# Performance work log

Hardware: AMD Instinct MI355X
Metric: run time of the kernel (lower is better)

The kernel has to match this reference:

```python
import jax, jax.numpy as jnp
import numpy as np

B, T, C = 4, 2048, 1024
H = 16                      # n_head
D = C // H                  # head dim = 64
FF = 4 * C                  # 4096


def setup_inputs() -> dict:
    key = jax.random.key(0)
    ks = jax.random.split(key, 9)
    s = 0.02
    return {
        "x": jax.random.normal(ks[0], (B, T, C), dtype=jnp.float32),
        # LayerNorm params (elementwise affine, default torch init)
        "ln1_w": jnp.ones((C,), jnp.float32),
        "ln1_b": jnp.zeros((C,), jnp.float32),
        "ln2_w": jnp.ones((C,), jnp.float32),
        "ln2_b": jnp.zeros((C,), jnp.float32),
        # attention weights, torch Linear layout [out, in], bias=False
        "w_attn": jax.random.normal(ks[1], (3 * C, C), jnp.float32) * s,
        "w_proj": jax.random.normal(ks[2], (C, C), jnp.float32) * s,
        # FFN weights
        "w_fc": jax.random.normal(ks[3], (FF, C), jnp.float32) * s,
        "w_fc_proj": jax.random.normal(ks[4], (C, FF), jnp.float32) * s,
    }


def _layernorm(x, w, b, eps=1e-5):
    mu = jnp.mean(x, axis=-1, keepdims=True)
    var = jnp.var(x, axis=-1, keepdims=True)
    return (x - mu) * jax.lax.rsqrt(var + eps) * w + b


def _attn(h, w_attn, w_proj):
    qkv = jnp.einsum('btc,fc->btf', h, w_attn)        # [B,T,3C]
    q, k, v = jnp.split(qkv, 3, axis=-1)
    q = q.reshape(B, T, H, D).transpose(0, 2, 1, 3)   # [B,H,T,D]
    k = k.reshape(B, T, H, D).transpose(0, 2, 1, 3)
    v = v.reshape(B, T, H, D).transpose(0, 2, 1, 3)
    att = jnp.einsum('bhtd,bhsd->bhts', q, k) * (1.0 / np.sqrt(D))
    causal = jnp.tril(jnp.ones((T, T), dtype=bool))
    att = jnp.where(causal, att, -jnp.inf)
    att = jax.nn.softmax(att, axis=-1)
    y = jnp.einsum('bhts,bhsd->bhtd', att, v)         # [B,H,T,D]
    y = y.transpose(0, 2, 1, 3).reshape(B, T, C)
    return jnp.einsum('btc,oc->bto', y, w_proj)


def _ffn(h, w_fc, w_fc_proj):
    u = jax.nn.gelu(jnp.einsum('btc,fc->btf', h, w_fc), approximate=False)
    return jnp.einsum('btf,cf->btc', u, w_fc_proj)


def reference(x, ln1_w, ln1_b, ln2_w, ln2_b, w_attn, w_proj, w_fc, w_fc_proj):
    x = x + _attn(_layernorm(x, ln1_w, ln1_b), w_attn, w_proj)
    x = x + _ffn(_layernorm(x, ln2_w, ln2_b), w_fc, w_fc_proj)
    return x
```

## Files before the change

### kernel.cpp

```cpp
#include <hip/hip_runtime.h>
#include <hip/hip_bf16.h>

using bf16 = __hip_bfloat16;
typedef __attribute__((ext_vector_type(8))) short short8;
typedef __attribute__((ext_vector_type(4))) short sh4;
typedef __attribute__((ext_vector_type(4))) float f32x4;

#define B_ 4
#define T_ 2048
#define C_ 1024
#define H_ 16
#define FF_ 4096
#define M_TOK (B_ * T_)
#define SCALE2 0.1803368801111f

#define BARRIER() asm volatile("s_barrier" ::: "memory")
#define WAITLGKM0() asm volatile("s_waitcnt lgkmcnt(0)" ::: "memory")
#define WAITLGKM8() asm volatile("s_waitcnt lgkmcnt(8)" ::: "memory")
#define WAITVM4() asm volatile("s_waitcnt vmcnt(4)" ::: "memory")
#define WAITVM2() asm volatile("s_waitcnt vmcnt(2)" ::: "memory")
#define WAITVM0() asm volatile("s_waitcnt vmcnt(0)" ::: "memory")

__device__ __forceinline__ void gload16(const void* g, void* l) {
    __builtin_amdgcn_global_load_lds(
        (const __attribute__((address_space(1))) void*)g,
        (__attribute__((address_space(3))) void*)l, 16, 0, 0);
}

__device__ __forceinline__ float fexp2(float x) {
    float r;
    asm("v_exp_f32 %0, %1" : "=v"(r) : "v"(x));
    return r;
}

__device__ __forceinline__ float bf16bits2f(short s) {
    return __uint_as_float(((unsigned)(unsigned short)s) << 16);
}

template <int CTRL>
__device__ __forceinline__ float dpp_rotf(float x) {
    return __int_as_float(__builtin_amdgcn_update_dpp(
        0, __float_as_int(x), CTRL, 0xf, 0xf, true));
}
__device__ __forceinline__ float red16_max(float v) {
    v = fmaxf(v, dpp_rotf<0x128>(v));
    v = fmaxf(v, dpp_rotf<0x124>(v));
    v = fmaxf(v, dpp_rotf<0x122>(v));
    v = fmaxf(v, dpp_rotf<0x121>(v));
    return v;
}
__device__ __forceinline__ float red16_sum(float v) {
    v += dpp_rotf<0x128>(v);
    v += dpp_rotf<0x124>(v);
    v += dpp_rotf<0x122>(v);
    v += dpp_rotf<0x121>(v);
    return v;
}

__global__ void cvt_f32_bf16_v4(const float* __restrict__ in, bf16* __restrict__ out, int n4) {
    int i = blockIdx.x * blockDim.x + threadIdx.x;
    if (i < n4) {
        float4 v = ((const float4*)in)[i];
        sh4 o;
        bf16 b0 = __float2bfloat16(v.x), b1 = __float2bfloat16(v.y),
             b2 = __float2bfloat16(v.z), b3 = __float2bfloat16(v.w);
        o[0] = *(short*)&b0; o[1] = *(short*)&b1;
        o[2] = *(short*)&b2; o[3] = *(short*)&b3;
        ((sh4*)out)[i] = o;
    }
}

template <typename TIN>
__global__ __launch_bounds__(256) void ln_kernel(const TIN* __restrict__ x,
                                                 const float* __restrict__ w,
                                                 const float* __restrict__ b,
                                                 bf16* __restrict__ out) {
    int row = blockIdx.x;
    int t = threadIdx.x;
    float4 v;
    if constexpr (sizeof(TIN) == 4) {
        v = ((const float4*)(x + (size_t)row * C_))[t];
    } else {
        sh4 h = ((const sh4*)(x + (size_t)row * C_))[t];
        v.x = bf16bits2f(h[0]);
        v.y = bf16bits2f(h[1]);
        v.z = bf16bits2f(h[2]);
        v.w = bf16bits2f(h[3]);
    }
    float s = v.x + v.y + v.z + v.w;
    float s2 = v.x * v.x + v.y * v.y + v.z * v.z + v.w * v.w;
#pragma unroll
    for (int off = 32; off > 0; off >>= 1) {
        s += __shfl_down(s, off);
        s2 += __shfl_down(s2, off);
    }
    __shared__ float ss[4], ss2[4];
    int wave = t >> 6, lane = t & 63;
    if (lane == 0) { ss[wave] = s; ss2[wave] = s2; }
    __syncthreads();
    s = ss[0] + ss[1] + ss[2] + ss[3];
    s2 = ss2[0] + ss2[1] + ss2[2] + ss2[3];
    float mu = s * (1.f / C_);
    float var = s2 * (1.f / C_) - mu * mu;
    float rstd = rsqrtf(var + 1e-5f);
    float4 wv = ((const float4*)w)[t];
    float4 bv = ((const float4*)b)[t];
    sh4 o;
    bf16 b0 = __float2bfloat16((v.x - mu) * rstd * wv.x + bv.x);
    bf16 b1 = __float2bfloat16((v.y - mu) * rstd * wv.y + bv.y);
    bf16 b2 = __float2bfloat16((v.z - mu) * rstd * wv.z + bv.z);
    bf16 b3 = __float2bfloat16((v.w - mu) * rstd * wv.w + bv.w);
    o[0] = *(short*)&b0; o[1] = *(short*)&b1;
    o[2] = *(short*)&b2; o[3] = *(short*)&b3;
    ((sh4*)(out + (size_t)row * C_))[t] = o;
}

#define STG(ldsbase, g, grow0, k0)                                               \
    {                                                                            \
        _Pragma("unroll") for (int s_ = 0; s_ < 2; s_++) {                       \
            int row_ = s_ * 64 + wid * 8 + sr;                                   \
            gload16(g + (size_t)((grow0) + row_) * K + (k0) + ssc,               \
                    (ldsbase) + row_ * 64 + (lane & 7) * 8);                     \
        }                                                                        \
    }

#define HALF256 (128 * 64)
template <int EPI>
__global__ __launch_bounds__(512, 2) void gemm256(const bf16* __restrict__ Ag,
                                                  const bf16* __restrict__ Bg,
                                                  void* __restrict__ Cout,
                                                  int M, int N, int K) {
    __shared__ short SA[2][256 * 64];
    __shared__ short SB[2][256 * 64];

    const int nbx = N >> 8;
    const int nwg = nbx * (M >> 8);
    const int bid = blockIdx.x;
    const int cpx = nwg >> 3;
    const int swzb = (bid & 7) * cpx + (bid >> 3);
    const int m0 = (swzb / nbx) * 256;
    const int n0 = (swzb % nbx) * 256;

    const int t = threadIdx.x;
    const int wid = t >> 6, lane = t & 63;
    const int wm = wid >> 2, wn = wid & 3;
    const int lrow = lane & 15, lg = lane >> 4;
    const int swzr = (lane & 7) * 8;
    const int sr = lane >> 3;
    const int ssc = ((lane & 7) ^ sr) * 8;

    f32x4 acc[8][4];
#pragma unroll
    for (int mi = 0; mi < 8; mi++)
#pragma unroll
        for (int ni = 0; ni < 4; ni++) acc[mi][ni] = (f32x4){0.f, 0.f, 0.f, 0.f};
    short8 bfr[4][2];

    const int T = K >> 6;
    const int niter = T >> 1;

#define DSREADS256(q, buf)                                                       \
    if ((q) == 0) {                                                              \
        _Pragma("unroll") for (int ni = 0; ni < 4; ni++)                         \
        _Pragma("unroll") for (int ks = 0; ks < 2; ks++)                         \
            bfr[ni][ks] = *(const short8*)(&SB[buf][(wn * 64 + ni * 16 + lrow) * 64 + \
                                                    ((ks * 32 + lg * 8) ^ swzr)]);    \
    }                                                                            \
    _Pragma("unroll") for (int mi2 = 0; mi2 < 2; mi2++)                          \
    _Pragma("unroll") for (int ks = 0; ks < 2; ks++)                             \
        af[mi2 * 2 + ks] = *(const short8*)(&SA[buf][(wm * 128 + (2 * (q) + mi2) * 16 + lrow) * 64 + \
                                                     ((ks * 32 + lg * 8) ^ swzr)]);

#define MFMAS256(q)                                                              \
    __builtin_amdgcn_s_setprio(1);                                               \
    _Pragma("unroll") for (int ks = 0; ks < 2; ks++)                             \
    _Pragma("unroll") for (int ni = 0; ni < 4; ni++)                             \
    _Pragma("unroll") for (int mi2 = 0; mi2 < 2; mi2++)                          \
        acc[2 * (q) + mi2][ni] = __builtin_amdgcn_mfma_f32_16x16x32_bf16(        \
            af[mi2 * 2 + ks], bfr[ni][ks], acc[2 * (q) + mi2][ni], 0, 0, 0);     \
    __builtin_amdgcn_s_setprio(0);

    STG(&SA[0][0], Ag, m0, 0);
    STG(&SA[0][HALF256], Ag, m0 + 128, 0);
    STG(&SB[0][0], Bg, n0, 0);
    STG(&SB[0][HALF256], Bg, n0 + 128, 0);
    STG(&SB[1][0], Bg, n0, 64);
    STG(&SB[1][HALF256], Bg, n0 + 128, 64);
    WAITVM4();
    BARRIER();

    for (int iter = 0; iter < niter; iter++) {
        const int tt = 2 * iter;
        const int ka = (tt + 1) * 64, kb = (tt + 2) * 64, kc = (tt + 3) * 64;
        const bool s2 = (tt + 2 < T), s3 = (tt + 3 < T);
        const bool last = (iter == niter - 1);
        short8 af[4];

        DSREADS256(0, 0);
        STG(&SA[1][0], Ag, m0, ka);
        WAITLGKM8();
        BARRIER(); WAITLGKM0(); MFMAS256(0); BARRIER();
        DSREADS256(1, 0);
        STG(&SA[1][HALF256], Ag, m0 + 128, ka);
        BARRIER(); WAITLGKM0(); MFMAS256(1); BARRIER();
        DSREADS256(2, 0);
        if (s2) STG(&SB[0][0], Bg, n0, kb);
        BARRIER(); WAITLGKM0(); MFMAS256(2); BARRIER();
        DSREADS256(3, 0);
        if (s2) STG(&SB[0][HALF256], Bg, n0 + 128, kb);
        BARRIER(); WAITLGKM0(); MFMAS256(3);
        if (last) { WAITVM0(); } else { WAITVM4(); }
        BARRIER();
        DSREADS256(0, 1);
        if (s2) STG(&SA[0][0], Ag, m0, kb);
        WAITLGKM8();
        BARRIER(); WAITLGKM0(); MFMAS256(0); BARRIER();
        DSREADS256(1, 1);
        if (s2) STG(&SA[0][HALF256], Ag, m0 + 128, kb);
        BARRIER(); WAITLGKM0(); MFMAS256(1); BARRIER();
        DSREADS256(2, 1);
        if (s3) STG(&SB[1][0], Bg, n0, kc);
        BARRIER(); WAITLGKM0(); MFMAS256(2); BARRIER();
        DSREADS256(3, 1);
        if (s3) STG(&SB[1][HALF256], Bg, n0 + 128, kc);
        BARRIER(); WAITLGKM0(); MFMAS256(3);
        if (!last) WAITVM4();
        BARRIER();
    }

#pragma unroll
    for (int mi = 0; mi < 8; mi++) {
#pragma unroll
        for (int ni = 0; ni < 4; ni++) {
            int gr = m0 + wm * 128 + mi * 16 + lg * 4;
            int gc = n0 + wn * 64 + ni * 16 + lrow;
#pragma unroll
            for (int r = 0; r < 4; r++) {
                size_t gi = (size_t)(gr + r) * N + gc;
                float v = acc[mi][ni][r];
                if constexpr (EPI == 0) {
                    ((bf16*)Cout)[gi] = __float2bfloat16(v);
                } else if constexpr (EPI == 5) {
                    float vv = (gc < C_) ? v * SCALE2 : v;
                    ((bf16*)Cout)[gi] = __float2bfloat16(vv);
                } else {
                    float ge = 0.5f * v * (1.f + erff(v * 0.70710678f));
                    ((bf16*)Cout)[gi] = __float2bfloat16(ge);
                }
            }
        }
    }
}

template <int EPI>
__global__ __launch_bounds__(512, 2) void gemm256x128(const bf16* __restrict__ Ag,
                                                      const bf16* __restrict__ Bg,
                                                      void* __restrict__ Cout,
                                                      const void* __restrict__ Res,
                                                      int M, int N, int K) {
    __shared__ short SA[2][256 * 64];
    __shared__ short SB[2][128 * 64];

    const int nbx = N >> 7;
    const int nwg = nbx * (M >> 8);
    const int bid = blockIdx.x;
    const int cpx = nwg >> 3;
    const int swzb = (bid & 7) * cpx + (bid >> 3);
    const int m0 = (swzb / nbx) * 256;
    const int n0 = (swzb % nbx) * 128;

    const int t = threadIdx.x;
    const int wid = t >> 6, lane = t & 63;
    const int wm = wid >> 1, wn = wid & 1;
    const int lrow = lane & 15, lg = lane >> 4;
    const int swzr = (lane & 7) * 8;
    const int sr = lane >> 3;
    const int ssc = ((lane & 7) ^ sr) * 8;

    f32x4 acc[4][4];
#pragma unroll
    for (int mi = 0; mi < 4; mi++)
#pragma unroll
        for (int ni = 0; ni < 4; ni++) acc[mi][ni] = (f32x4){0.f, 0.f, 0.f, 0.f};
    short8 bfr[4][2];

    const int T = K >> 6;
    const int niter = T >> 1;

#define DSRX(p, buf)                                                             \
    if ((p) == 0) {                                                              \
        _Pragma("unroll") for (int ni = 0; ni < 4; ni++)                         \
        _Pragma("unroll") for (int ks = 0; ks < 2; ks++)                         \
            bfr[ni][ks] = *(const short8*)(&SB[buf][(wn * 64 + ni * 16 + lrow) * 64 + \
                                                    ((ks * 32 + lg * 8) ^ swzr)]);    \
    }                                                                            \
    _Pragma("unroll") for (int mi2 = 0; mi2 < 2; mi2++)                          \
    _Pragma("unroll") for (int ks = 0; ks < 2; ks++)                             \
        af[mi2 * 2 + ks] = *(const short8*)(&SA[buf][(wm * 64 + (2 * (p) + mi2) * 16 + lrow) * 64 + \
                                                     ((ks * 32 + lg * 8) ^ swzr)]);

#define MFX(p)                                                                   \
    __builtin_amdgcn_s_setprio(1);                                               \
    _Pragma("unroll") for (int ks = 0; ks < 2; ks++)                             \
    _Pragma("unroll") for (int ni = 0; ni < 4; ni++)                             \
    _Pragma("unroll") for (int mi2 = 0; mi2 < 2; mi2++)                          \
        acc[2 * (p) + mi2][ni] = __builtin_amdgcn_mfma_f32_16x16x32_bf16(        \
            af[mi2 * 2 + ks], bfr[ni][ks], acc[2 * (p) + mi2][ni], 0, 0, 0);     \
    __builtin_amdgcn_s_setprio(0);

    STG(&SA[0][0], Ag, m0, 0);
    STG(&SA[0][HALF256], Ag, m0 + 128, 0);
    STG(&SB[0][0], Bg, n0, 0);
    STG(&SB[1][0], Bg, n0, 64);
    WAITVM2();
    BARRIER();

    for (int iter = 0; iter < niter; iter++) {
        const int tt = 2 * iter;
        const int ka = (tt + 1) * 64, kb = (tt + 2) * 64, kc = (tt + 3) * 64;
        const bool s2 = (tt + 2 < T), s3 = (tt + 3 < T);
        const bool last = (iter == niter - 1);
        short8 af[4];

        DSRX(0, 0);
        STG(&SA[1][0], Ag, m0, ka);
        STG(&SA[1][HALF256], Ag, m0 + 128, ka);
        WAITLGKM8();
        BARRIER(); WAITLGKM0(); MFX(0); BARRIER();
        DSRX(1, 0);
        if (s2) STG(&SB[0][0], Bg, n0, kb);
        BARRIER(); WAITLGKM0(); MFX(1);
        if (last) { WAITVM0(); } else { WAITVM2(); }
        BARRIER();
        DSRX(0, 1);
        if (s2) {
            STG(&SA[0][0], Ag, m0, kb);
            STG(&SA[0][HALF256], Ag, m0 + 128, kb);
        }
        WAITLGKM8();
        BARRIER(); WAITLGKM0(); MFX(0); BARRIER();
        DSRX(1, 1);
        if (s3) STG(&SB[1][0], Bg, n0, kc);
        BARRIER(); WAITLGKM0(); MFX(1);
        if (last) { WAITVM0(); } else { WAITVM2(); }
        BARRIER();
    }

#pragma unroll
    for (int mi = 0; mi < 4; mi++) {
#pragma unroll
        for (int ni = 0; ni < 4; ni++) {
            int gr = m0 + wm * 64 + mi * 16 + lg * 4;
            int gc = n0 + wn * 64 + ni * 16 + lrow;
#pragma unroll
            for (int r = 0; r < 4; r++) {
                size_t gi = (size_t)(gr + r) * N + gc;
                float v = acc[mi][ni][r];
                if constexpr (EPI == 0) {
                    ((bf16*)Cout)[gi] = __float2bfloat16(v);
                } else if constexpr (EPI == 3) {
                    float res = ((const float*)Res)[gi];
                    ((bf16*)Cout)[gi] = __float2bfloat16(res + v);
                } else {
                    float res = __bfloat162float(((const bf16*)Res)[gi]);
                    ((float*)Cout)[gi] = res + v;
                }
            }
        }
    }
}

__global__ __launch_bounds__(256, 4) void flash_attn(const bf16* __restrict__ qk,
                                                     const bf16* __restrict__ vt,
                                                     bf16* __restrict__ y) {
    const int pi = blockIdx.x;
    const int bh = blockIdx.y;
    const int b = bh >> 4, h = bh & 15;
    const int t = threadIdx.x;
    const int wave = t >> 6, lane = t & 63;
    const int lrow = lane & 15, g = lane >> 4, lk = g * 8;

    __shared__ alignas(16) short Ks[64 * 72];
    __shared__ alignas(16) short Vs[64 * 72];
    __shared__ alignas(16) short Ps[64 * 72];

    const size_t rs = 2 * C_;
    const bf16* Qg = qk + (size_t)b * T_ * rs + h * 64;
    const bf16* Kg = Qg + C_;
    const bf16* Vg = vt + (size_t)(h * 64) * M_TOK + b * T_;

    const int srow = t >> 3;
    const int sc8 = (t & 7) * 8;

    for (int sel = 0; sel < 2; sel++) {
        const int qtb = sel ? pi : 31 - pi;
        const int q0 = qtb * 64;
        const int nkt = qtb + 1;

        short8 qf[2];
        {
            const bf16* qr = Qg + (size_t)(q0 + wave * 16 + lrow) * rs;
            qf[0] = *(const short8*)(qr + lk);
            qf[1] = *(const short8*)(qr + 32 + lk);
        }

        f32x4 o[4];
        float m[4], l[4];
#pragma unroll
        for (int ni = 0; ni < 4; ni++) o[ni] = (f32x4){0.f, 0.f, 0.f, 0.f};
#pragma unroll
        for (int r = 0; r < 4; r++) { m[r] = -1e30f; l[r] = 0.f; }

        short8 kr[2], vr[2];
#pragma unroll
        for (int p = 0; p < 2; p++) {
            int r = srow + p * 32;
            kr[p] = *(const short8*)(Kg + (size_t)r * rs + sc8);
            vr[p] = *(const short8*)(Vg + (size_t)r * M_TOK + sc8);
        }

        for (int kt = 0; kt < nkt; kt++) {
            const int s0 = kt * 64;
#pragma unroll
            for (int p = 0; p < 2; p++) {
                int r = srow + p * 32;
                *(short8*)(&Ks[r * 72 + sc8]) = kr[p];
                *(short8*)(&Vs[r * 72 + sc8]) = vr[p];
            }
            __syncthreads();
            if (kt + 1 < nkt) {
                const int s0n = (kt + 1) * 64;
#pragma unroll
                for (int p = 0; p < 2; p++) {
                    int r = srow + p * 32;
                    kr[p] = *(const short8*)(Kg + (size_t)(s0n + r) * rs + sc8);
                    vr[p] = *(const short8*)(Vg + (size_t)r * M_TOK + s0n + sc8);
                }
            }

            f32x4 s[4];
#pragma unroll
            for (int ni = 0; ni < 4; ni++) s[ni] = (f32x4){0.f, 0.f, 0.f, 0.f};
            __builtin_amdgcn_s_setprio(1);
#pragma unroll
            for (int ks = 0; ks < 2; ks++) {
#pragma unroll
                for (int ni = 0; ni < 4; ni++) {
                    short8 kf = *(const short8*)(&Ks[(ni * 16 + lrow) * 72 + ks * 32 + lk]);
                    s[ni] = __builtin_amdgcn_mfma_f32_16x16x32_bf16(qf[ks], kf, s[ni], 0, 0, 0);
                }
            }
            __builtin_amdgcn_s_setprio(0);

            if (kt == nkt - 1) {
#pragma unroll
                for (int ni = 0; ni < 4; ni++)
#pragma unroll
                    for (int r = 0; r < 4; r++) {
                        int qg = q0 + wave * 16 + g * 4 + r;
                        int kvg = s0 + ni * 16 + lrow;
                        if (kvg > qg) s[ni][r] = -1e30f;
                    }
            }

            float pm[4];
#pragma unroll
            for (int r = 0; r < 4; r++) {
                float v = fmaxf(fmaxf(s[0][r], s[1][r]), fmaxf(s[2][r], s[3][r]));
                pm[r] = red16_max(v);
            }
            float dmax = fmaxf(fmaxf(pm[0] - m[0], pm[1] - m[1]),
                               fmaxf(pm[2] - m[2], pm[3] - m[3]));
            if (!__all(dmax <= 8.f)) {
                float alpha[4];
#pragma unroll
                for (int r = 0; r < 4; r++) {
                    float mn = fmaxf(m[r], pm[r]);
                    alpha[r] = fexp2(m[r] - mn);
                    m[r] = mn;
                    l[r] *= alpha[r];
                }
#pragma unroll
                for (int ni = 0; ni < 4; ni++)
#pragma unroll
                    for (int r = 0; r < 4; r++) o[ni][r] *= alpha[r];
            }
            float rowsum[4] = {0.f, 0.f, 0.f, 0.f};
#pragma unroll
            for (int ni = 0; ni < 4; ni++) {
#pragma unroll
                for (int r = 0; r < 4; r++) {
                    float p = fexp2(s[ni][r] - m[r]);
                    rowsum[r] += p;
                    bf16 pb = __float2bfloat16(p);
                    Ps[(wave * 16 + g * 4 + r) * 72 + ni * 16 + lrow] = *(short*)&pb;
                }
            }
#pragma unroll
            for (int r = 0; r < 4; r++)
                l[r] += red16_sum(rowsum[r]);

            __builtin_amdgcn_s_setprio(1);
#pragma unroll
            for (int ks2 = 0; ks2 < 2; ks2++) {
                short8 pf = *(const short8*)(&Ps[(wave * 16 + lrow) * 72 + ks2 * 32 + lk]);
#pragma unroll
                for (int ni = 0; ni < 4; ni++) {
                    short8 vf = *(const short8*)(&Vs[(ni * 16 + lrow) * 72 + ks2 * 32 + lk]);
                    o[ni] = __builtin_amdgcn_mfma_f32_16x16x32_bf16(pf, vf, o[ni], 0, 0, 0);
                }
            }
            __builtin_amdgcn_s_setprio(0);
            __syncthreads();
        }

        float inv[4];
#pragma unroll
        for (int r = 0; r < 4; r++) inv[r] = 1.f / l[r];
#pragma unroll
        for (int ni = 0; ni < 4; ni++)
#pragma unroll
            for (int r = 0; r < 4; r++) {
                int qrow = q0 + wave * 16 + g * 4 + r;
                y[((size_t)(b * T_ + qrow)) * C_ + h * 64 + ni * 16 + lrow] =
                    __float2bfloat16(o[ni][r] * inv[r]);
            }
    }
}

extern "C" void kernel_launch(void* const* d_in, const int* in_sizes, int n_in,
                              void* d_out, int out_size, void* d_ws, size_t ws_size,
                              hipStream_t stream) {
    const float* x      = (const float*)d_in[0];
    const float* ln1w   = (const float*)d_in[1];
    const float* ln1b   = (const float*)d_in[2];
    const float* ln2w   = (const float*)d_in[3];
    const float* ln2b   = (const float*)d_in[4];
    const float* w_attn = (const float*)d_in[5];
    const float* w_proj = (const float*)d_in[6];
    const float* w_fc   = (const float*)d_in[7];
    const float* w_fcp  = (const float*)d_in[8];
    float* out = (float*)d_out;

    char* ws = (char*)d_ws;
    bf16* ln_buf  = (bf16*)(ws);
    bf16* qk_buf  = (bf16*)(ws + (16u << 20));
    bf16* vt_buf  = (bf16*)(ws + (48u << 20));
    bf16* ybuf    = (bf16*)(ws + (64u << 20));
    bf16* ubuf    = (bf16*)(ws + (16u << 20));
    bf16* x2b     = (bf16*)(ws + (80u << 20));
    bf16* wattn_h = (bf16*)(ws + (112u << 20));
    bf16* wproj_h = (bf16*)(ws + (118u << 20));
    bf16* wfc_h   = (bf16*)(ws + (120u << 20));
    bf16* wfcp_h  = (bf16*)(ws + (128u << 20));

    {
        int n1 = 3 * C_ * C_ / 4, n2 = C_ * C_ / 4, n3 = FF_ * C_ / 4, n4 = C_ * FF_ / 4;
        cvt_f32_bf16_v4<<<(n1 + 255) / 256, 256, 0, stream>>>(w_attn, wattn_h, n1);
        cvt_f32_bf16_v4<<<(n2 + 255) / 256, 256, 0, stream>>>(w_proj, wproj_h, n2);
        cvt_f32_bf16_v4<<<(n3 + 255) / 256, 256, 0, stream>>>(w_fc, wfc_h, n3);
        cvt_f32_bf16_v4<<<(n4 + 255) / 256, 256, 0, stream>>>(w_fcp, wfcp_h, n4);
    }

    ln_kernel<float><<<M_TOK, 256, 0, stream>>>(x, ln1w, ln1b, ln_buf);

    gemm256<5><<<dim3((M_TOK / 256) * (2 * C_ / 256)), 512, 0, stream>>>(
        ln_buf, wattn_h, qk_buf, M_TOK, 2 * C_, C_);

    gemm256x128<0><<<dim3((C_ / 256) * (M_TOK / 128)), 512, 0, stream>>>(
        wattn_h + (size_t)2 * C_ * C_, ln_buf, vt_buf, nullptr, C_, M_TOK, C_);

    flash_attn<<<dim3(16, B_ * H_), 256, 0, stream>>>(qk_buf, vt_buf, ybuf);

    gemm256x128<3><<<dim3((M_TOK / 256) * (C_ / 128)), 512, 0, stream>>>(
        ybuf, wproj_h, x2b, x, M_TOK, C_, C_);

    ln_kernel<bf16><<<M_TOK, 256, 0, stream>>>(x2b, ln2w, ln2b, ln_buf);

    gemm256<2><<<dim3((M_TOK / 256) * (FF_ / 256)), 512, 0, stream>>>(
        ln_buf, wfc_h, ubuf, M_TOK, FF_, C_);

    gemm256x128<4><<<dim3((M_TOK / 256) * (C_ / 128)), 512, 0, stream>>>(
        ubuf, wfcp_h, out, x2b, M_TOK, C_, FF_);
}
```

Before: 382.2 us.

## Swap MFMA operands for transposed accumulators and vectorize epilogue stores

Swaps the A/B operands of every MFMA in the GEMMs and attention so each lane's four accumulator registers hold consecutive columns of one row rather than four rows of one column. GEMM epilogues and attention output can then write packed 8-byte bf16 stores (and vector residual loads) instead of scalar 2-byte stores. In attention, each lane now owns a single query row, so the softmax max and sum become per-lane reductions plus two cross-lane shuffles instead of per-row DPP reductions, and P is written to LDS in packed form. The cost is a different register/fragment mapping that must stay consistent with the LDS read patterns, and the shuffles go through the LDS crossbar rather than DPP.

```diff
diff --git a/kernel.cpp b/kernel.cpp
--- a/kernel.cpp
+++ b/kernel.cpp
@@ -37,36 +37,20 @@
     return __uint_as_float(((unsigned)(unsigned short)s) << 16);
 }
 
-template <int CTRL>
-__device__ __forceinline__ float dpp_rotf(float x) {
-    return __int_as_float(__builtin_amdgcn_update_dpp(
-        0, __float_as_int(x), CTRL, 0xf, 0xf, true));
-}
-__device__ __forceinline__ float red16_max(float v) {
-    v = fmaxf(v, dpp_rotf<0x128>(v));
-    v = fmaxf(v, dpp_rotf<0x124>(v));
-    v = fmaxf(v, dpp_rotf<0x122>(v));
-    v = fmaxf(v, dpp_rotf<0x121>(v));
-    return v;
-}
-__device__ __forceinline__ float red16_sum(float v) {
-    v += dpp_rotf<0x128>(v);
-    v += dpp_rotf<0x124>(v);
-    v += dpp_rotf<0x122>(v);
-    v += dpp_rotf<0x121>(v);
-    return v;
+__device__ __forceinline__ unsigned bf2(float a, float b) {
+    bf16 x = __float2bfloat16(a), y = __float2bfloat16(b);
+    unsigned short ux = *(unsigned short*)&x, uy = *(unsigned short*)&y;
+    return (unsigned)ux | ((unsigned)uy << 16);
 }
 
 __global__ void cvt_f32_bf16_v4(const float* __restrict__ in, bf16* __restrict__ out, int n4) {
     int i = blockIdx.x * blockDim.x + threadIdx.x;
     if (i < n4) {
         float4 v = ((const float4*)in)[i];
-        sh4 o;
-        bf16 b0 = __float2bfloat16(v.x), b1 = __float2bfloat16(v.y),
-             b2 = __float2bfloat16(v.z), b3 = __float2bfloat16(v.w);
-        o[0] = *(short*)&b0; o[1] = *(short*)&b1;
-        o[2] = *(short*)&b2; o[3] = *(short*)&b3;
-        ((sh4*)out)[i] = o;
+        uint2 o;
+        o.x = bf2(v.x, v.y);
+        o.y = bf2(v.z, v.w);
+        ((uint2*)out)[i] = o;
     }
 }
 
@@ -105,14 +89,10 @@
     float rstd = rsqrtf(var + 1e-5f);
     float4 wv = ((const float4*)w)[t];
     float4 bv = ((const float4*)b)[t];
-    sh4 o;
-    bf16 b0 = __float2bfloat16((v.x - mu) * rstd * wv.x + bv.x);
-    bf16 b1 = __float2bfloat16((v.y - mu) * rstd * wv.y + bv.y);
-    bf16 b2 = __float2bfloat16((v.z - mu) * rstd * wv.z + bv.z);
-    bf16 b3 = __float2bfloat16((v.w - mu) * rstd * wv.w + bv.w);
-    o[0] = *(short*)&b0; o[1] = *(short*)&b1;
-    o[2] = *(short*)&b2; o[3] = *(short*)&b3;
-    ((sh4*)(out + (size_t)row * C_))[t] = o;
+    uint2 o;
+    o.x = bf2((v.x - mu) * rstd * wv.x + bv.x, (v.y - mu) * rstd * wv.y + bv.y);
+    o.y = bf2((v.z - mu) * rstd * wv.z + bv.z, (v.w - mu) * rstd * wv.w + bv.w);
+    ((uint2*)(out + (size_t)row * C_))[t] = o;
 }
 
 #define STG(ldsbase, g, grow0, k0)                                               \
@@ -177,7 +157,7 @@
     _Pragma("unroll") for (int ni = 0; ni < 4; ni++)                             \
     _Pragma("unroll") for (int mi2 = 0; mi2 < 2; mi2++)                          \
         acc[2 * (q) + mi2][ni] = __builtin_amdgcn_mfma_f32_16x16x32_bf16(        \
-            af[mi2 * 2 + ks], bfr[ni][ks], acc[2 * (q) + mi2][ni], 0, 0, 0);     \
+            bfr[ni][ks], af[mi2 * 2 + ks], acc[2 * (q) + mi2][ni], 0, 0, 0);     \
     __builtin_amdgcn_s_setprio(0);
 
     STG(&SA[0][0], Ag, m0, 0);
@@ -230,23 +210,26 @@
 
 #pragma unroll
     for (int mi = 0; mi < 8; mi++) {
+        const int gm = m0 + wm * 128 + mi * 16 + lrow;
 #pragma unroll
         for (int ni = 0; ni < 4; ni++) {
-            int gr = m0 + wm * 128 + mi * 16 + lg * 4;
-            int gc = n0 + wn * 64 + ni * 16 + lrow;
-#pragma unroll
-            for (int r = 0; r < 4; r++) {
-                size_t gi = (size_t)(gr + r) * N + gc;
-                float v = acc[mi][ni][r];
-                if constexpr (EPI == 0) {
-                    ((bf16*)Cout)[gi] = __float2bfloat16(v);
-                } else if constexpr (EPI == 5) {
-                    float vv = (gc < C_) ? v * SCALE2 : v;
-                    ((bf16*)Cout)[gi] = __float2bfloat16(vv);
-                } else {
-                    float ge = 0.5f * v * (1.f + erff(v * 0.70710678f));
-                    ((bf16*)Cout)[gi] = __float2bfloat16(ge);
-                }
+            const int gn = n0 + wn * 64 + ni * 16 + lg * 4;
+            size_t gi = (size_t)gm * N + gn;
+            f32x4 a = acc[mi][ni];
+            if constexpr (EPI == 0) {
+                uint2 o; o.x = bf2(a[0], a[1]); o.y = bf2(a[2], a[3]);
+                *(uint2*)&(((bf16*)Cout)[gi]) = o;
+            } else if constexpr (EPI == 5) {
+                float sc = (gn < C_) ? SCALE2 : 1.f;
+                uint2 o; o.x = bf2(a[0] * sc, a[1] * sc); o.y = bf2(a[2] * sc, a[3] * sc);
+                *(uint2*)&(((bf16*)Cout)[gi]) = o;
+            } else {
+                float g0 = 0.5f * a[0] * (1.f + erff(a[0] * 0.70710678f));
+                float g1 = 0.5f * a[1] * (1.f + erff(a[1] * 0.70710678f));
+                float g2 = 0.5f * a[2] * (1.f + erff(a[2] * 0.70710678f));
+                float g3 = 0.5f * a[3] * (1.f + erff(a[3] * 0.70710678f));
+                uint2 o; o.x = bf2(g0, g1); o.y = bf2(g2, g3);
+                *(uint2*)&(((bf16*)Cout)[gi]) = o;
             }
         }
     }
@@ -305,7 +288,7 @@
     _Pragma("unroll") for (int ni = 0; ni < 4; ni++)                             \
     _Pragma("unroll") for (int mi2 = 0; mi2 < 2; mi2++)                          \
         acc[2 * (p) + mi2][ni] = __builtin_amdgcn_mfma_f32_16x16x32_bf16(        \
-            af[mi2 * 2 + ks], bfr[ni][ks], acc[2 * (p) + mi2][ni], 0, 0, 0);     \
+            bfr[ni][ks], af[mi2 * 2 + ks], acc[2 * (p) + mi2][ni], 0, 0, 0);     \
     __builtin_amdgcn_s_setprio(0);
 
     STG(&SA[0][0], Ag, m0, 0);
@@ -348,23 +331,27 @@
 
 #pragma unroll
     for (int mi = 0; mi < 4; mi++) {
+        const int gm = m0 + wm * 64 + mi * 16 + lrow;
 #pragma unroll
         for (int ni = 0; ni < 4; ni++) {
-            int gr = m0 + wm * 64 + mi * 16 + lg * 4;
-            int gc = n0 + wn * 64 + ni * 16 + lrow;
-#pragma unroll
-            for (int r = 0; r < 4; r++) {
-                size_t gi = (size_t)(gr + r) * N + gc;
-                float v = acc[mi][ni][r];
-                if constexpr (EPI == 0) {
-                    ((bf16*)Cout)[gi] = __float2bfloat16(v);
-                } else if constexpr (EPI == 3) {
-                    float res = ((const float*)Res)[gi];
-                    ((bf16*)Cout)[gi] = __float2bfloat16(res + v);
-                } else {
-                    float res = __bfloat162float(((const bf16*)Res)[gi]);
-                    ((float*)Cout)[gi] = res + v;
-                }
+            const int gn = n0 + wn * 64 + ni * 16 + lg * 4;
+            size_t gi = (size_t)gm * N + gn;
+            f32x4 a = acc[mi][ni];
+            if constexpr (EPI == 0) {
+                uint2 o; o.x = bf2(a[0], a[1]); o.y = bf2(a[2], a[3]);
+                *(uint2*)&(((bf16*)Cout)[gi]) = o;
+            } else if constexpr (EPI == 3) {
+                float4 rv = *(const float4*)&(((const float*)Res)[gi]);
+                uint2 o; o.x = bf2(rv.x + a[0], rv.y + a[1]); o.y = bf2(rv.z + a[2], rv.w + a[3]);
+                *(uint2*)&(((bf16*)Cout)[gi]) = o;
+            } else {
+                sh4 hv = *(const sh4*)&(((const bf16*)Res)[gi]);
+                float4 o;
+                o.x = bf16bits2f(hv[0]) + a[0];
+                o.y = bf16bits2f(hv[1]) + a[1];
+                o.z = bf16bits2f(hv[2]) + a[2];
+                o.w = bf16bits2f(hv[3]) + a[3];
+                *(float4*)&(((float*)Cout)[gi]) = o;
             }
         }
     }
@@ -378,7 +365,7 @@
     const int b = bh >> 4, h = bh & 15;
     const int t = threadIdx.x;
     const int wave = t >> 6, lane = t & 63;
-    const int lrow = lane & 15, g = lane >> 4, lk = g * 8;
+    const int lrow = lane & 15, lg = lane >> 4, lk = lg * 8;
 
     __shared__ alignas(16) short Ks[64 * 72];
     __shared__ alignas(16) short Vs[64 * 72];
@@ -396,20 +383,19 @@
         const int qtb = sel ? pi : 31 - pi;
         const int q0 = qtb * 64;
         const int nkt = qtb + 1;
+        const int qg = q0 + wave * 16 + lrow;
 
         short8 qf[2];
         {
-            const bf16* qr = Qg + (size_t)(q0 + wave * 16 + lrow) * rs;
+            const bf16* qr = Qg + (size_t)qg * rs;
             qf[0] = *(const short8*)(qr + lk);
             qf[1] = *(const short8*)(qr + 32 + lk);
         }
 
         f32x4 o[4];
-        float m[4], l[4];
+        float m1 = -1e30f, l1 = 0.f;
 #pragma unroll
         for (int ni = 0; ni < 4; ni++) o[ni] = (f32x4){0.f, 0.f, 0.f, 0.f};
-#pragma unroll
-        for (int r = 0; r < 4; r++) { m[r] = -1e30f; l[r] = 0.f; }
 
         short8 kr[2], vr[2];
 #pragma unroll
@@ -447,7 +433,7 @@
 #pragma unroll
                 for (int ni = 0; ni < 4; ni++) {
                     short8 kf = *(const short8*)(&Ks[(ni * 16 + lrow) * 72 + ks * 32 + lk]);
-                    s[ni] = __builtin_amdgcn_mfma_f32_16x16x32_bf16(qf[ks], kf, s[ni], 0, 0, 0);
+                    s[ni] = __builtin_amdgcn_mfma_f32_16x16x32_bf16(kf, qf[ks], s[ni], 0, 0, 0);
                 }
             }
             __builtin_amdgcn_s_setprio(0);
@@ -457,48 +443,42 @@
                 for (int ni = 0; ni < 4; ni++)
 #pragma unroll
                     for (int r = 0; r < 4; r++) {
-                        int qg = q0 + wave * 16 + g * 4 + r;
-                        int kvg = s0 + ni * 16 + lrow;
+                        int kvg = s0 + ni * 16 + lg * 4 + r;
                         if (kvg > qg) s[ni][r] = -1e30f;
                     }
             }
 
-            float pm[4];
-#pragma unroll
-            for (int r = 0; r < 4; r++) {
-                float v = fmaxf(fmaxf(s[0][r], s[1][r]), fmaxf(s[2][r], s[3][r]));
-                pm[r] = red16_max(v);
-            }
-            float dmax = fmaxf(fmaxf(pm[0] - m[0], pm[1] - m[1]),
-                               fmaxf(pm[2] - m[2], pm[3] - m[3]));
-            if (!__all(dmax <= 8.f)) {
-                float alpha[4];
-#pragma unroll
-                for (int r = 0; r < 4; r++) {
-                    float mn = fmaxf(m[r], pm[r]);
-                    alpha[r] = fexp2(m[r] - mn);
-                    m[r] = mn;
-                    l[r] *= alpha[r];
-                }
+            float pm = s[0][0];
+#pragma unroll
+            for (int ni = 0; ni < 4; ni++)
+#pragma unroll
+                for (int r = 0; r < 4; r++) pm = fmaxf(pm, s[ni][r]);
+            pm = fmaxf(pm, __shfl_xor(pm, 16));
+            pm = fmaxf(pm, __shfl_xor(pm, 32));
+            if (!__all(pm - m1 <= 8.f)) {
+                float mn = fmaxf(m1, pm);
+                float alpha = fexp2(m1 - mn);
+                m1 = mn;
+                l1 *= alpha;
 #pragma unroll
                 for (int ni = 0; ni < 4; ni++)
 #pragma unroll
-                    for (int r = 0; r < 4; r++) o[ni][r] *= alpha[r];
-            }
-            float rowsum[4] = {0.f, 0.f, 0.f, 0.f};
+                    for (int r = 0; r < 4; r++) o[ni][r] *= alpha;
+            }
+            float rsum = 0.f;
 #pragma unroll
             for (int ni = 0; ni < 4; ni++) {
-#pragma unroll
-                for (int r = 0; r < 4; r++) {
-                    float p = fexp2(s[ni][r] - m[r]);
-                    rowsum[r] += p;
-                    bf16 pb = __float2bfloat16(p);
-                    Ps[(wave * 16 + g * 4 + r) * 72 + ni * 16 + lrow] = *(short*)&pb;
-                }
-            }
-#pragma unroll
-            for (int r = 0; r < 4; r++)
-                l[r] += red16_sum(rowsum[r]);
+                float p0 = fexp2(s[ni][0] - m1);
+                float p1 = fexp2(s[ni][1] - m1);
+                float p2 = fexp2(s[ni][2] - m1);
+                float p3 = fexp2(s[ni][3] - m1);
+                rsum += (p0 + p1) + (p2 + p3);
+                uint2 pk; pk.x = bf2(p0, p1); pk.y = bf2(p2, p3);
+                *(uint2*)(&Ps[(wave * 16 + lrow) * 72 + ni * 16 + lg * 4]) = pk;
+            }
+            rsum += __shfl_xor(rsum, 16);
+            rsum += __shfl_xor(rsum, 32);
+            l1 += rsum;
 
             __builtin_amdgcn_s_setprio(1);
 #pragma unroll
@@ -507,24 +487,21 @@
 #pragma unroll
                 for (int ni = 0; ni < 4; ni++) {
                     short8 vf = *(const short8*)(&Vs[(ni * 16 + lrow) * 72 + ks2 * 32 + lk]);
-                    o[ni] = __builtin_amdgcn_mfma_f32_16x16x32_bf16(pf, vf, o[ni], 0, 0, 0);
+                    o[ni] = __builtin_amdgcn_mfma_f32_16x16x32_bf16(vf, pf, o[ni], 0, 0, 0);
                 }
             }
             __builtin_amdgcn_s_setprio(0);
             __syncthreads();
         }
 
-        float inv[4];
-#pragma unroll
-        for (int r = 0; r < 4; r++) inv[r] = 1.f / l[r];
-#pragma unroll
-        for (int ni = 0; ni < 4; ni++)
-#pragma unroll
-            for (int r = 0; r < 4; r++) {
-                int qrow = q0 + wave * 16 + g * 4 + r;
-                y[((size_t)(b * T_ + qrow)) * C_ + h * 64 + ni * 16 + lrow] =
-                    __float2bfloat16(o[ni][r] * inv[r]);
-            }
+        float inv = 1.f / l1;
+#pragma unroll
+        for (int ni = 0; ni < 4; ni++) {
+            uint2 pk;
+            pk.x = bf2(o[ni][0] * inv, o[ni][1] * inv);
+            pk.y = bf2(o[ni][2] * inv, o[ni][3] * inv);
+            *(uint2*)(&y[((size_t)(b * T_ + qg)) * C_ + h * 64 + ni * 16 + lg * 4]) = pk;
+        }
     }
 }
 
```

New measurement: 382.1 us. No clear change (-0.0%).
